# Kernel tuning notes

Hardware: AMD Instinct MI355X
Metric: run time of the kernel (lower is better)

## Reference

```python
import jax, jax.numpy as jnp
import numpy as np

N, T, D, H = 4, 2048, 512, 8
HD = D // H  # head dim = split size


def setup_inputs() -> dict:
    key = jax.random.key(0)
    k1, k2, k3, k4 = jax.random.split(key, 4)
    scale = 1.0 / np.sqrt(D)
    return {
        "query": jax.random.normal(k1, (N, T, D), dtype=jnp.float32),
        "Wk": jax.random.normal(k2, (D, D), dtype=jnp.float32) * scale,
        "Wv": jax.random.normal(k3, (D, D), dtype=jnp.float32) * scale,
        "Wo": jax.random.normal(k4, (D, D), dtype=jnp.float32) * scale,
    }


def reference(query, Wk, Wv, Wo):
    # torch.nn.Linear(x) == x @ W.T (no bias)
    querys = query                              # [N, T, D]
    keys = query @ Wk.T + query                 # residual-added keys [N, T, D]
    values = query @ Wv.T                       # [N, T, D]

    # split along feature dim into H heads, stacked on a leading head axis
    def split_heads(x):
        # [N, T, D] -> [H, N, T, HD]
        return jnp.transpose(x.reshape(N, T, H, HD), (2, 0, 1, 3))

    q = split_heads(querys)
    k = split_heads(keys)
    v = split_heads(values)

    scores = jnp.einsum("hnqd,hnkd->hnqk", q, k) / np.sqrt(HD).astype(np.float32)
    scores = jax.nn.softmax(scores, axis=3)      # [H, N, Tq, Tk]
    out = jnp.einsum("hnqk,hnkd->hnqd", scores, v)

    # concat heads back along feature dim: [H, N, T, HD] -> [N, T, D]
    out = jnp.transpose(out, (1, 2, 0, 3)).reshape(N, T, D)
    out = out @ Wo.T
    return out
```

## Files before the change

### kernel.cpp

```cpp
#include <hip/hip_runtime.h>
#include <cstdint>
#include <cstddef>

#define NB 4
#define TS 2048
#define DM 512
#define HN 8
#define HD 64

typedef __attribute__((ext_vector_type(8))) short bf16x8;
typedef __attribute__((ext_vector_type(16))) float f32x16;
typedef __attribute__((ext_vector_type(4))) float f32x4;
typedef __attribute__((ext_vector_type(4))) short short4v;
typedef __attribute__((ext_vector_type(4))) unsigned u32x4;

static __device__ __forceinline__ short f2bf(float f) {
  unsigned u = __float_as_uint(f);
  unsigned r = (u + 0x7fffu + ((u >> 16) & 1u)) >> 16;
  return (short)r;
}

static __device__ __forceinline__ float bf2f(short s) {
  return __uint_as_float(((unsigned)(unsigned short)s) << 16);
}

static __device__ __forceinline__ unsigned cvtpk(float lo, float hi) {
  unsigned r;
  asm("v_cvt_pk_bf16_f32 %0, %1, %2" : "=v"(r) : "v"(lo), "v"(hi));
  return r;
}

static __device__ __forceinline__ void plane32swap(unsigned& x, unsigned& y) {
  asm volatile("v_permlane32_swap_b32 %0, %1" : "+v"(x), "+v"(y));
}

static __device__ __forceinline__ void gload16(const void* g, void* l) {
  __builtin_amdgcn_global_load_lds(
      (const __attribute__((address_space(1))) void*)g,
      (__attribute__((address_space(3))) void*)l, 16, 0, 0);
}

#define WAIT_VM(N) asm volatile("s_waitcnt vmcnt(" #N ")" ::: "memory")
#define BAR() __builtin_amdgcn_s_barrier()

#define MFMA16(a, b, c) __builtin_amdgcn_mfma_f32_16x16x32_bf16((a), (b), (c), 0, 0, 0)
#define MFMA32(a, b, c) __builtin_amdgcn_mfma_f32_32x32x16_bf16((a), (b), (c), 0, 0, 0)

__global__ __launch_bounds__(256) void cast_all(const float* __restrict__ Q,
                                                const float* __restrict__ Wk,
                                                const float* __restrict__ Wv,
                                                const float* __restrict__ Wo,
                                                short* __restrict__ Qb,
                                                short* __restrict__ Wb) {
  int i = blockIdx.x * 256 + threadIdx.x;
  const int Q4 = (NB * TS * DM) / 4;
  const float* src;
  short* dst;
  int off;
  int which = -1;
  if (i < Q4) {
    src = Q; dst = Qb; off = i;
  } else {
    int j = i - Q4;
    which = j >> 16;
    off = j & 65535;
    src = which == 0 ? Wk : (which == 1 ? Wv : Wo);
    dst = Wb + ((size_t)which << 18);
  }
  float4 v = reinterpret_cast<const float4*>(src)[off];
  if (which == 0) {
    int e0 = off * 4;
    int row = e0 >> 9;
    int col0 = e0 & 511;
    if (row >= col0 && row < col0 + 4) {
      int c = row - col0;
      if (c == 0) v.x += 1.0f;
      else if (c == 1) v.y += 1.0f;
      else if (c == 2) v.z += 1.0f;
      else v.w += 1.0f;
    }
  }
  short4v o;
  o.x = f2bf(v.x);
  o.y = f2bf(v.y);
  o.z = f2bf(v.z);
  o.w = f2bf(v.w);
  reinterpret_cast<short4v*>(dst)[off] = o;
}

__global__ __launch_bounds__(256) void gemm_kv(const short* __restrict__ Qb,
                                               const short* __restrict__ Wkb,
                                               const short* __restrict__ Wvb,
                                               short* __restrict__ KP,
                                               short* __restrict__ VP) {
  __shared__ alignas(16) short lA[2][128 * 32];
  __shared__ alignas(16) short lK[2][64 * 32];
  __shared__ alignas(16) short lV[2][64 * 32];
  const int row0 = blockIdx.x * 128;
  const int col0d = blockIdx.y * 64;
  const int tid = threadIdx.x;
  const int lane = tid & 63;
  const int wave = tid >> 6;
  const int wr = wave >> 1, wc = wave & 1;
  const int fr = lane & 15, fk = (lane >> 4) * 8;
  const int g = lane >> 4;

  f32x4 kacc[2][4], vacc[4][2];
  const f32x4 z4 = {0.f, 0.f, 0.f, 0.f};
#pragma unroll
  for (int m = 0; m < 4; ++m)
#pragma unroll
    for (int nn = 0; nn < 2; ++nn) {
      kacc[nn][m] = z4;
      vacc[m][nn] = z4;
    }

  const int sr = tid >> 2;
  const int sc8 = (tid & 3) * 8;

#define GSTAGE(buf, kt)                                                 \
  do {                                                                  \
    gload16(&Qb[(size_t)(row0 + sr) * DM + (kt) + sc8],                 \
            (char*)&lA[(buf)][0] + (size_t)tid * 16);                   \
    gload16(&Qb[(size_t)(row0 + 64 + sr) * DM + (kt) + sc8],            \
            (char*)&lA[(buf)][0] + 4096 + (size_t)tid * 16);            \
    gload16(&Wkb[(size_t)(col0d + sr) * DM + (kt) + sc8],               \
            (char*)&lK[(buf)][0] + (size_t)tid * 16);                   \
    gload16(&Wvb[(size_t)(col0d + sr) * DM + (kt) + sc8],               \
            (char*)&lV[(buf)][0] + (size_t)tid * 16);                   \
  } while (0)

  GSTAGE(0, 0);
  __syncthreads();
  int cur = 0;
  for (int kt = 0; kt < 16; ++kt) {
    if (kt < 15) GSTAGE(cur ^ 1, (kt + 1) * 32);
    bf16x8 af[4], wk[2], wv[2];
#pragma unroll
    for (int m = 0; m < 4; ++m)
      af[m] = *reinterpret_cast<const bf16x8*>(&lA[cur][(wr * 64 + m * 16 + fr) * 32 + fk]);
#pragma unroll
    for (int nn = 0; nn < 2; ++nn) {
      wk[nn] = *reinterpret_cast<const bf16x8*>(&lK[cur][(wc * 32 + nn * 16 + fr) * 32 + fk]);
      wv[nn] = *reinterpret_cast<const bf16x8*>(&lV[cur][(wc * 32 + nn * 16 + fr) * 32 + fk]);
    }
    __builtin_amdgcn_s_setprio(1);
#pragma unroll
    for (int m = 0; m < 4; ++m)
#pragma unroll
      for (int nn = 0; nn < 2; ++nn) {
        kacc[nn][m] = MFMA16(wk[nn], af[m], kacc[nn][m]);
        vacc[m][nn] = MFMA16(af[m], wv[nn], vacc[m][nn]);
      }
    __builtin_amdgcn_s_setprio(0);
    __syncthreads();
    cur ^= 1;
  }
#undef GSTAGE

#pragma unroll
  for (int nn = 0; nn < 2; ++nn) {
#pragma unroll
    for (int m = 0; m < 4; ++m) {
      int d = col0d + wc * 32 + nn * 16 + g * 4;
      int kseq = row0 + wr * 64 + m * 16 + fr;
      int h = d >> 6, dd = d & 63;
      int n = kseq >> 11, kk = kseq & (TS - 1);
      int t = kk >> 6, H = (kk >> 5) & 1;
      int ks = (dd >> 4) & 3, hfd = (dd >> 3) & 1, jb = dd & 7;
      int slot = (kk & 31) + 32 * hfd;
      short4v pk;
#pragma unroll
      for (int i = 0; i < 4; ++i) pk[i] = f2bf(kacc[nn][m][i]);
      size_t addr = ((((size_t)(n * HN + h) * 32 + t) * 8 + H * 4 + ks) * 64 + slot) * 8 + jb;
      *reinterpret_cast<short4v*>(&KP[addr]) = pk;
    }
  }
#pragma unroll
  for (int m = 0; m < 4; ++m) {
#pragma unroll
    for (int nn = 0; nn < 2; ++nn) {
      int kseq = row0 + wr * 64 + m * 16 + g * 4;
      int d = col0d + wc * 32 + nn * 16 + fr;
      int h = d >> 6, dd = d & 63;
      int n = kseq >> 11, kk = kseq & (TS - 1);
      int t = kk >> 6, hfk = (kk >> 3) & 1, jb = kk & 7;
      int ksV = (kk >> 4) & 3, D = (dd >> 5) & 1;
      int slot = (dd & 31) + 32 * hfk;
      short4v pv;
#pragma unroll
      for (int i = 0; i < 4; ++i) pv[i] = f2bf(vacc[m][nn][i]);
      size_t addr = ((((size_t)(n * HN + h) * 32 + t) * 8 + D * 4 + ksV) * 64 + slot) * 8 + jb;
      *reinterpret_cast<short4v*>(&VP[addr]) = pv;
    }
  }
}

__global__ __launch_bounds__(256) void gemm_o(const short* __restrict__ A,
                                              const short* __restrict__ W,
                                              float* __restrict__ out0) {
  __shared__ alignas(16) short lA[2][128 * 32];
  __shared__ alignas(16) short lB[2][64 * 32];
  const int row0 = blockIdx.x * 128;
  const int col0 = blockIdx.y * 64;
  const int tid = threadIdx.x;
  const int lane = tid & 63;
  const int wave = tid >> 6;
  const int wr = wave >> 1, wc = wave & 1;
  const int fr = lane & 15, fk = (lane >> 4) * 8;

  f32x4 acc[4][2];
  const f32x4 z4 = {0.f, 0.f, 0.f, 0.f};
#pragma unroll
  for (int m = 0; m < 4; ++m)
#pragma unroll
    for (int nn = 0; nn < 2; ++nn) acc[m][nn] = z4;

  const int sr = tid >> 2;
  const int sc8 = (tid & 3) * 8;

#define GSTAGE(buf, kt)                                                \
  do {                                                                 \
    gload16(&A[(size_t)(row0 + sr) * DM + (kt) + sc8],                 \
            (char*)&lA[(buf)][0] + (size_t)tid * 16);                  \
    gload16(&A[(size_t)(row0 + 64 + sr) * DM + (kt) + sc8],            \
            (char*)&lA[(buf)][0] + 4096 + (size_t)tid * 16);           \
    gload16(&W[(size_t)(col0 + sr) * DM + (kt) + sc8],                 \
            (char*)&lB[(buf)][0] + (size_t)tid * 16);                  \
  } while (0)

  GSTAGE(0, 0);
  __syncthreads();
  int cur = 0;
  for (int kt = 0; kt < 16; ++kt) {
    if (kt < 15) GSTAGE(cur ^ 1, (kt + 1) * 32);
    bf16x8 af[4], bfr[2];
#pragma unroll
    for (int m = 0; m < 4; ++m)
      af[m] = *reinterpret_cast<const bf16x8*>(&lA[cur][(wr * 64 + m * 16 + fr) * 32 + fk]);
#pragma unroll
    for (int nn = 0; nn < 2; ++nn)
      bfr[nn] = *reinterpret_cast<const bf16x8*>(&lB[cur][(wc * 32 + nn * 16 + fr) * 32 + fk]);
    __builtin_amdgcn_s_setprio(1);
#pragma unroll
    for (int m = 0; m < 4; ++m)
#pragma unroll
      for (int nn = 0; nn < 2; ++nn) acc[m][nn] = MFMA16(af[m], bfr[nn], acc[m][nn]);
    __builtin_amdgcn_s_setprio(0);
    __syncthreads();
    cur ^= 1;
  }
#undef GSTAGE

#pragma unroll
  for (int m = 0; m < 4; ++m)
#pragma unroll
    for (int nn = 0; nn < 2; ++nn)
#pragma unroll
      for (int i = 0; i < 4; ++i) {
        int gr = row0 + wr * 64 + m * 16 + (lane >> 4) * 4 + i;
        int gc = col0 + wc * 32 + nn * 16 + fr;
        out0[(size_t)gr * DM + gc] = acc[m][nn][i];
      }
}

__global__ __launch_bounds__(512, 4) void attn(const short* __restrict__ Qb,
                                               const short* __restrict__ KP,
                                               const short* __restrict__ VP,
                                               short* __restrict__ Ob) {
  __shared__ alignas(16) short kv[2][2][2][64 * 64];
  const int bid = blockIdx.x;
  const int blk = (bid & 7) * 64 + (bid >> 3);
  const int qt = blk & 15;
  const int nh = blk >> 4;
  const int h = nh & (HN - 1);
  const int n = nh >> 3;
  const int wv = threadIdx.x >> 6, lane = threadIdx.x & 63;
  const int grp = wv >> 2, qs = wv & 3;
  const int l31 = lane & 31, hf = lane >> 5;
  const int q0 = qt * 128 + qs * 32;
  const float SC2 = 0.18033688011f;

  bf16x8 qf[4];
  const short* qrow = Qb + (size_t)(n * TS + q0 + l31) * DM + h * HD;
#pragma unroll
  for (int ks = 0; ks < 4; ++ks) {
    bf16x8 t = *reinterpret_cast<const bf16x8*>(qrow + ks * 16 + hf * 8);
#pragma unroll
    for (int j = 0; j < 8; ++j) t[j] = f2bf(bf2f(t[j]) * SC2);
    qf[ks] = t;
  }

  bf16x8 ones;
#pragma unroll
  for (int i = 0; i < 8; ++i) ones[i] = (short)0x3F80;

  f32x16 o0, o1, osum;
#pragma unroll
  for (int r = 0; r < 16; ++r) {
    o0[r] = 0.f;
    o1[r] = 0.f;
    osum[r] = 0.f;
  }

  const int tbase = grp * 16;
  const size_t nhbase = (size_t)nh * 32 * 4096;

#define STAGE(buf, t)                                                           \
  do {                                                                          \
    const short* kS = KP + nhbase + (size_t)(t) * 4096 + qs * 1024 + lane * 8;  \
    const short* vS = VP + nhbase + (size_t)(t) * 4096 + qs * 1024 + lane * 8;  \
    char* kb_ = (char*)&kv[grp][(buf)][0][0] + qs * 2048;                       \
    char* vb_ = (char*)&kv[grp][(buf)][1][0] + qs * 2048;                       \
    gload16(kS, kb_);                                                           \
    gload16(kS + 512, kb_ + 1024);                                              \
    gload16(vS, vb_);                                                           \
    gload16(vS + 512, vb_ + 1024);                                              \
  } while (0)

  STAGE(0, tbase);

  const int lb = lane * 16;
  int cur = 0;
  for (int j = 0; j < 16; ++j) {
    if (j < 15) {
      STAGE(cur ^ 1, tbase + j + 1);
      WAIT_VM(4);
    } else {
      WAIT_VM(0);
    }
    BAR();

    const char* Kl = (const char*)&kv[grp][cur][0][0];
    const char* Vl = (const char*)&kv[grp][cur][1][0];

    f32x16 s0, s1;
#pragma unroll
    for (int r = 0; r < 16; ++r) {
      s0[r] = 0.f;
      s1[r] = 0.f;
    }
    __builtin_amdgcn_s_setprio(1);
#pragma unroll
    for (int ks = 0; ks < 4; ++ks) {
      bf16x8 ka0 = *reinterpret_cast<const bf16x8*>(Kl + ks * 1024 + lb);
      bf16x8 ka1 = *reinterpret_cast<const bf16x8*>(Kl + (4 + ks) * 1024 + lb);
      s0 = MFMA32(ka0, qf[ks], s0);
      s1 = MFMA32(ka1, qf[ks], s1);
    }
    __builtin_amdgcn_s_setprio(0);

#pragma unroll
    for (int r = 0; r < 16; ++r) {
      s0[r] = __builtin_amdgcn_exp2f(s0[r]);
      s1[r] = __builtin_amdgcn_exp2f(s1[r]);
    }

    unsigned w0[4][2], w1[4][2];
#pragma unroll
    for (int c = 0; c < 4; ++c) {
      w0[c][0] = cvtpk(s0[4 * c], s0[4 * c + 1]);
      w0[c][1] = cvtpk(s0[4 * c + 2], s0[4 * c + 3]);
      w1[c][0] = cvtpk(s1[4 * c], s1[4 * c + 1]);
      w1[c][1] = cvtpk(s1[4 * c + 2], s1[4 * c + 3]);
    }

    __builtin_amdgcn_s_setprio(1);
#pragma unroll
    for (int ks = 0; ks < 4; ++ks) {
      const int ce = (ks & 1) * 2, co = ce + 1;
      unsigned xa = (ks < 2) ? w0[ce][0] : w1[ce][0];
      unsigned xb = (ks < 2) ? w0[ce][1] : w1[ce][1];
      unsigned ya = (ks < 2) ? w0[co][0] : w1[co][0];
      unsigned yb = (ks < 2) ? w0[co][1] : w1[co][1];
      plane32swap(xa, ya);
      plane32swap(xb, yb);
      u32x4 pw;
      pw.x = xa;
      pw.y = xb;
      pw.z = ya;
      pw.w = yb;
      bf16x8 pa = *reinterpret_cast<bf16x8*>(&pw);

      bf16x8 v0 = *reinterpret_cast<const bf16x8*>(Vl + ks * 1024 + lb);
      bf16x8 v1 = *reinterpret_cast<const bf16x8*>(Vl + (4 + ks) * 1024 + lb);
      o0 = MFMA32(pa, v0, o0);
      o1 = MFMA32(pa, v1, o1);
      osum = MFMA32(pa, ones, osum);
    }
    __builtin_amdgcn_s_setprio(0);

    BAR();
    cur ^= 1;
  }
#undef STAGE

  float* sp = (float*)&kv[0][0][0][0];
  const int sbase = (qs * 64 + lane) * 49;
  if (grp == 1) {
#pragma unroll
    for (int r = 0; r < 16; ++r) {
      sp[sbase + r] = o0[r];
      sp[sbase + 16 + r] = o1[r];
      sp[sbase + 32 + r] = osum[r];
    }
  }
  __syncthreads();
  if (grp == 0) {
#pragma unroll
    for (int r = 0; r < 16; ++r) {
      o0[r] += sp[sbase + r];
      o1[r] += sp[sbase + 16 + r];
      osum[r] += sp[sbase + 32 + r];
    }
#pragma unroll
    for (int r = 0; r < 16; ++r) {
      int q = q0 + (r & 3) + 8 * (r >> 2) + 4 * hf;
      float is = 1.0f / osum[r];
      size_t base = (size_t)(n * TS + q) * DM + h * HD;
      Ob[base + l31] = f2bf(o0[r] * is);
      Ob[base + 32 + l31] = f2bf(o1[r] * is);
    }
  }
}

extern "C" void kernel_launch(void* const* d_in, const int* in_sizes, int n_in,
                              void* d_out, int out_size, void* d_ws, size_t ws_size,
                              hipStream_t stream) {
  (void)in_sizes; (void)n_in; (void)out_size; (void)ws_size;
  const float* Q = (const float*)d_in[0];
  const float* Wk = (const float*)d_in[1];
  const float* Wv = (const float*)d_in[2];
  const float* Wo = (const float*)d_in[3];

  const size_t QE = (size_t)NB * TS * DM;
  const size_t WE = (size_t)DM * DM;
  short* ws = (short*)d_ws;
  short* Qb = ws;
  short* KP = Qb + QE;
  short* VP = KP + QE;
  short* Ao = VP + QE;
  short* Wkb = Ao + QE;
  short* Wvb = Wkb + WE;
  short* Wob = Wvb + WE;

  {
    int total4 = (int)((QE + 3 * WE) / 4);
    cast_all<<<total4 / 256, 256, 0, stream>>>(Q, Wk, Wv, Wo, Qb, Wkb);
  }
  {
    dim3 g(64, 8);
    gemm_kv<<<g, 256, 0, stream>>>(Qb, Wkb, Wvb, KP, VP);
  }
  attn<<<NB * HN * (TS / 128), 512, 0, stream>>>(Qb, KP, VP, Ao);
  {
    dim3 g(64, 8);
    gemm_o<<<g, 256, 0, stream>>>(Ao, Wob, (float*)d_out);
  }
}
```

Before: 79.71 us.

## Halve row tiles in projection GEMMs and attention; single-buffer attention K/V

The K/V projection and output GEMMs now use 64-row tiles instead of 128-row tiles, which doubles their grid size. The attention kernel drops from 512 to 256 threads per block and covers 64 query rows per block instead of 128. Its K/V staging goes from a double-buffered prefetch to a single buffer that is loaded after each compute step. The goal is more blocks and lower LDS use per block, for better CU occupancy and balance. The cost is that K/V load latency is no longer overlapped with compute, and K/V and weight tiles are re-read more often from global memory.

```diff
diff --git a/kernel.cpp b/kernel.cpp
--- a/kernel.cpp
+++ b/kernel.cpp
@@ -93,10 +93,10 @@
                                                const short* __restrict__ Wvb,
                                                short* __restrict__ KP,
                                                short* __restrict__ VP) {
-  __shared__ alignas(16) short lA[2][128 * 32];
+  __shared__ alignas(16) short lA[2][64 * 32];
   __shared__ alignas(16) short lK[2][64 * 32];
   __shared__ alignas(16) short lV[2][64 * 32];
-  const int row0 = blockIdx.x * 128;
+  const int row0 = blockIdx.x * 64;
   const int col0d = blockIdx.y * 64;
   const int tid = threadIdx.x;
   const int lane = tid & 63;
@@ -105,10 +105,10 @@
   const int fr = lane & 15, fk = (lane >> 4) * 8;
   const int g = lane >> 4;
 
-  f32x4 kacc[2][4], vacc[4][2];
+  f32x4 kacc[2][2], vacc[2][2];
   const f32x4 z4 = {0.f, 0.f, 0.f, 0.f};
 #pragma unroll
-  for (int m = 0; m < 4; ++m)
+  for (int m = 0; m < 2; ++m)
 #pragma unroll
     for (int nn = 0; nn < 2; ++nn) {
       kacc[nn][m] = z4;
@@ -122,8 +122,6 @@
   do {                                                                  \
     gload16(&Qb[(size_t)(row0 + sr) * DM + (kt) + sc8],                 \
             (char*)&lA[(buf)][0] + (size_t)tid * 16);                   \
-    gload16(&Qb[(size_t)(row0 + 64 + sr) * DM + (kt) + sc8],            \
-            (char*)&lA[(buf)][0] + 4096 + (size_t)tid * 16);            \
     gload16(&Wkb[(size_t)(col0d + sr) * DM + (kt) + sc8],               \
             (char*)&lK[(buf)][0] + (size_t)tid * 16);                   \
     gload16(&Wvb[(size_t)(col0d + sr) * DM + (kt) + sc8],               \
@@ -135,10 +133,10 @@
   int cur = 0;
   for (int kt = 0; kt < 16; ++kt) {
     if (kt < 15) GSTAGE(cur ^ 1, (kt + 1) * 32);
-    bf16x8 af[4], wk[2], wv[2];
-#pragma unroll
-    for (int m = 0; m < 4; ++m)
-      af[m] = *reinterpret_cast<const bf16x8*>(&lA[cur][(wr * 64 + m * 16 + fr) * 32 + fk]);
+    bf16x8 af[2], wk[2], wv[2];
+#pragma unroll
+    for (int m = 0; m < 2; ++m)
+      af[m] = *reinterpret_cast<const bf16x8*>(&lA[cur][(wr * 32 + m * 16 + fr) * 32 + fk]);
 #pragma unroll
     for (int nn = 0; nn < 2; ++nn) {
       wk[nn] = *reinterpret_cast<const bf16x8*>(&lK[cur][(wc * 32 + nn * 16 + fr) * 32 + fk]);
@@ -146,7 +144,7 @@
     }
     __builtin_amdgcn_s_setprio(1);
 #pragma unroll
-    for (int m = 0; m < 4; ++m)
+    for (int m = 0; m < 2; ++m)
 #pragma unroll
       for (int nn = 0; nn < 2; ++nn) {
         kacc[nn][m] = MFMA16(wk[nn], af[m], kacc[nn][m]);
@@ -161,9 +159,9 @@
 #pragma unroll
   for (int nn = 0; nn < 2; ++nn) {
 #pragma unroll
-    for (int m = 0; m < 4; ++m) {
+    for (int m = 0; m < 2; ++m) {
       int d = col0d + wc * 32 + nn * 16 + g * 4;
-      int kseq = row0 + wr * 64 + m * 16 + fr;
+      int kseq = row0 + wr * 32 + m * 16 + fr;
       int h = d >> 6, dd = d & 63;
       int n = kseq >> 11, kk = kseq & (TS - 1);
       int t = kk >> 6, H = (kk >> 5) & 1;
@@ -177,10 +175,10 @@
     }
   }
 #pragma unroll
-  for (int m = 0; m < 4; ++m) {
+  for (int m = 0; m < 2; ++m) {
 #pragma unroll
     for (int nn = 0; nn < 2; ++nn) {
-      int kseq = row0 + wr * 64 + m * 16 + g * 4;
+      int kseq = row0 + wr * 32 + m * 16 + g * 4;
       int d = col0d + wc * 32 + nn * 16 + fr;
       int h = d >> 6, dd = d & 63;
       int n = kseq >> 11, kk = kseq & (TS - 1);
@@ -199,9 +197,9 @@
 __global__ __launch_bounds__(256) void gemm_o(const short* __restrict__ A,
                                               const short* __restrict__ W,
                                               float* __restrict__ out0) {
-  __shared__ alignas(16) short lA[2][128 * 32];
+  __shared__ alignas(16) short lA[2][64 * 32];
   __shared__ alignas(16) short lB[2][64 * 32];
-  const int row0 = blockIdx.x * 128;
+  const int row0 = blockIdx.x * 64;
   const int col0 = blockIdx.y * 64;
   const int tid = threadIdx.x;
   const int lane = tid & 63;
@@ -209,10 +207,10 @@
   const int wr = wave >> 1, wc = wave & 1;
   const int fr = lane & 15, fk = (lane >> 4) * 8;
 
-  f32x4 acc[4][2];
+  f32x4 acc[2][2];
   const f32x4 z4 = {0.f, 0.f, 0.f, 0.f};
 #pragma unroll
-  for (int m = 0; m < 4; ++m)
+  for (int m = 0; m < 2; ++m)
 #pragma unroll
     for (int nn = 0; nn < 2; ++nn) acc[m][nn] = z4;
 
@@ -223,8 +221,6 @@
   do {                                                                 \
     gload16(&A[(size_t)(row0 + sr) * DM + (kt) + sc8],                 \
             (char*)&lA[(buf)][0] + (size_t)tid * 16);                  \
-    gload16(&A[(size_t)(row0 + 64 + sr) * DM + (kt) + sc8],            \
-            (char*)&lA[(buf)][0] + 4096 + (size_t)tid * 16);           \
     gload16(&W[(size_t)(col0 + sr) * DM + (kt) + sc8],                 \
             (char*)&lB[(buf)][0] + (size_t)tid * 16);                  \
   } while (0)
@@ -234,16 +230,16 @@
   int cur = 0;
   for (int kt = 0; kt < 16; ++kt) {
     if (kt < 15) GSTAGE(cur ^ 1, (kt + 1) * 32);
-    bf16x8 af[4], bfr[2];
-#pragma unroll
-    for (int m = 0; m < 4; ++m)
-      af[m] = *reinterpret_cast<const bf16x8*>(&lA[cur][(wr * 64 + m * 16 + fr) * 32 + fk]);
+    bf16x8 af[2], bfr[2];
+#pragma unroll
+    for (int m = 0; m < 2; ++m)
+      af[m] = *reinterpret_cast<const bf16x8*>(&lA[cur][(wr * 32 + m * 16 + fr) * 32 + fk]);
 #pragma unroll
     for (int nn = 0; nn < 2; ++nn)
       bfr[nn] = *reinterpret_cast<const bf16x8*>(&lB[cur][(wc * 32 + nn * 16 + fr) * 32 + fk]);
     __builtin_amdgcn_s_setprio(1);
 #pragma unroll
-    for (int m = 0; m < 4; ++m)
+    for (int m = 0; m < 2; ++m)
 #pragma unroll
       for (int nn = 0; nn < 2; ++nn) acc[m][nn] = MFMA16(af[m], bfr[nn], acc[m][nn]);
     __builtin_amdgcn_s_setprio(0);
@@ -253,32 +249,32 @@
 #undef GSTAGE
 
 #pragma unroll
-  for (int m = 0; m < 4; ++m)
+  for (int m = 0; m < 2; ++m)
 #pragma unroll
     for (int nn = 0; nn < 2; ++nn)
 #pragma unroll
       for (int i = 0; i < 4; ++i) {
-        int gr = row0 + wr * 64 + m * 16 + (lane >> 4) * 4 + i;
+        int gr = row0 + wr * 32 + m * 16 + (lane >> 4) * 4 + i;
         int gc = col0 + wc * 32 + nn * 16 + fr;
         out0[(size_t)gr * DM + gc] = acc[m][nn][i];
       }
 }
 
-__global__ __launch_bounds__(512, 4) void attn(const short* __restrict__ Qb,
+__global__ __launch_bounds__(256, 4) void attn(const short* __restrict__ Qb,
                                                const short* __restrict__ KP,
                                                const short* __restrict__ VP,
                                                short* __restrict__ Ob) {
-  __shared__ alignas(16) short kv[2][2][2][64 * 64];
+  __shared__ alignas(16) short kv[2][2][4096];
   const int bid = blockIdx.x;
-  const int blk = (bid & 7) * 64 + (bid >> 3);
-  const int qt = blk & 15;
-  const int nh = blk >> 4;
+  const int blk = (bid & 7) * 128 + (bid >> 3);
+  const int qt = blk & 31;
+  const int nh = blk >> 5;
   const int h = nh & (HN - 1);
   const int n = nh >> 3;
   const int wv = threadIdx.x >> 6, lane = threadIdx.x & 63;
-  const int grp = wv >> 2, qs = wv & 3;
+  const int grp = wv >> 1, qs = wv & 1;
   const int l31 = lane & 31, hf = lane >> 5;
-  const int q0 = qt * 128 + qs * 32;
+  const int q0 = qt * 64 + qs * 32;
   const float SC2 = 0.18033688011f;
 
   bf16x8 qf[4];
@@ -306,33 +302,31 @@
   const int tbase = grp * 16;
   const size_t nhbase = (size_t)nh * 32 * 4096;
 
-#define STAGE(buf, t)                                                           \
+#define STAGE(t)                                                                \
   do {                                                                          \
-    const short* kS = KP + nhbase + (size_t)(t) * 4096 + qs * 1024 + lane * 8;  \
-    const short* vS = VP + nhbase + (size_t)(t) * 4096 + qs * 1024 + lane * 8;  \
-    char* kb_ = (char*)&kv[grp][(buf)][0][0] + qs * 2048;                       \
-    char* vb_ = (char*)&kv[grp][(buf)][1][0] + qs * 2048;                       \
+    const short* kS = KP + nhbase + (size_t)(t) * 4096 + qs * 2048 + lane * 8;  \
+    const short* vS = VP + nhbase + (size_t)(t) * 4096 + qs * 2048 + lane * 8;  \
+    char* kb_ = (char*)&kv[grp][0][0] + qs * 4096;                              \
+    char* vb_ = (char*)&kv[grp][1][0] + qs * 4096;                              \
     gload16(kS, kb_);                                                           \
     gload16(kS + 512, kb_ + 1024);                                              \
+    gload16(kS + 1024, kb_ + 2048);                                             \
+    gload16(kS + 1536, kb_ + 3072);                                             \
     gload16(vS, vb_);                                                           \
     gload16(vS + 512, vb_ + 1024);                                              \
+    gload16(vS + 1024, vb_ + 2048);                                             \
+    gload16(vS + 1536, vb_ + 3072);                                             \
   } while (0)
 
-  STAGE(0, tbase);
+  STAGE(tbase);
 
   const int lb = lane * 16;
-  int cur = 0;
   for (int j = 0; j < 16; ++j) {
-    if (j < 15) {
-      STAGE(cur ^ 1, tbase + j + 1);
-      WAIT_VM(4);
-    } else {
-      WAIT_VM(0);
-    }
+    WAIT_VM(0);
     BAR();
 
-    const char* Kl = (const char*)&kv[grp][cur][0][0];
-    const char* Vl = (const char*)&kv[grp][cur][1][0];
+    const char* Kl = (const char*)&kv[grp][0][0];
+    const char* Vl = (const char*)&kv[grp][1][0];
 
     f32x16 s0, s1;
 #pragma unroll
@@ -391,11 +385,11 @@
     __builtin_amdgcn_s_setprio(0);
 
     BAR();
-    cur ^= 1;
+    if (j < 15) STAGE(tbase + j + 1);
   }
 #undef STAGE
 
-  float* sp = (float*)&kv[0][0][0][0];
+  float* sp = (float*)&kv[0][0][0];
   const int sbase = (qs * 64 + lane) * 49;
   if (grp == 1) {
 #pragma unroll
@@ -449,12 +443,12 @@
     cast_all<<<total4 / 256, 256, 0, stream>>>(Q, Wk, Wv, Wo, Qb, Wkb);
   }
   {
-    dim3 g(64, 8);
+    dim3 g(128, 8);
     gemm_kv<<<g, 256, 0, stream>>>(Qb, Wkb, Wvb, KP, VP);
   }
-  attn<<<NB * HN * (TS / 128), 512, 0, stream>>>(Qb, KP, VP, Ao);
+  attn<<<NB * HN * (TS / 64), 256, 0, stream>>>(Qb, KP, VP, Ao);
   {
-    dim3 g(64, 8);
+    dim3 g(128, 8);
     gemm_o<<<g, 256, 0, stream>>>(Ao, Wob, (float*)d_out);
   }
 }
```

Result: slower. 87.31 us (+9.5%).

## Software-pipeline attention loop: overlap QK of next tile with PV of previous

Applied to the files above, without the earlier changes.

Restructures the attention inner loop so that each iteration computes QK^T for tile j while doing the PV product for tile j-1 using probabilities packed in the previous iteration. K and V are now staged separately with staggered prefetch, K one tile ahead and V aligned to the PV step, and the LDS buffers are reindexed accordingly. The aim is to let the exp/pack work overlap with MFMA work and to shorten the dependency chain between QK, softmax and PV. This adds a prologue and epilogue, keeps more live registers (cw arrays and s0/s1 across iterations), and makes the vmcnt wait counts more delicate.

```diff
diff --git a/kernel.cpp b/kernel.cpp
--- a/kernel.cpp
+++ b/kernel.cpp
@@ -268,7 +268,7 @@
                                                const short* __restrict__ KP,
                                                const short* __restrict__ VP,
                                                short* __restrict__ Ob) {
-  __shared__ alignas(16) short kv[2][2][2][64 * 64];
+  __shared__ alignas(16) short kv[2][2][2][4096];
   const int bid = blockIdx.x;
   const int blk = (bid & 7) * 64 + (bid >> 3);
   const int qt = blk & 15;
@@ -295,105 +295,128 @@
 #pragma unroll
   for (int i = 0; i < 8; ++i) ones[i] = (short)0x3F80;
 
-  f32x16 o0, o1, osum;
+  f32x16 o0, o1, osum, s0, s1;
 #pragma unroll
   for (int r = 0; r < 16; ++r) {
     o0[r] = 0.f;
     o1[r] = 0.f;
     osum[r] = 0.f;
   }
+  unsigned cw0[4][2], cw1[4][2];
 
   const int tbase = grp * 16;
   const size_t nhbase = (size_t)nh * 32 * 4096;
-
-#define STAGE(buf, t)                                                           \
-  do {                                                                          \
-    const short* kS = KP + nhbase + (size_t)(t) * 4096 + qs * 1024 + lane * 8;  \
-    const short* vS = VP + nhbase + (size_t)(t) * 4096 + qs * 1024 + lane * 8;  \
-    char* kb_ = (char*)&kv[grp][(buf)][0][0] + qs * 2048;                       \
-    char* vb_ = (char*)&kv[grp][(buf)][1][0] + qs * 2048;                       \
-    gload16(kS, kb_);                                                           \
-    gload16(kS + 512, kb_ + 1024);                                              \
-    gload16(vS, vb_);                                                           \
-    gload16(vS + 512, vb_ + 1024);                                              \
-  } while (0)
-
-  STAGE(0, tbase);
-
   const int lb = lane * 16;
-  int cur = 0;
-  for (int j = 0; j < 16; ++j) {
-    if (j < 15) {
-      STAGE(cur ^ 1, tbase + j + 1);
-      WAIT_VM(4);
-    } else {
-      WAIT_VM(0);
-    }
+
+#define STAGE_K(buf, t)                                                          \
+  do {                                                                           \
+    const short* kS = KP + nhbase + (size_t)(t) * 4096 + qs * 1024 + lane * 8;   \
+    char* kb_ = (char*)&kv[grp][0][(buf)][0] + qs * 2048;                        \
+    gload16(kS, kb_);                                                            \
+    gload16(kS + 512, kb_ + 1024);                                               \
+  } while (0)
+
+#define STAGE_V(buf, t)                                                          \
+  do {                                                                           \
+    const short* vS = VP + nhbase + (size_t)(t) * 4096 + qs * 1024 + lane * 8;   \
+    char* vb_ = (char*)&kv[grp][1][(buf)][0] + qs * 2048;                        \
+    gload16(vS, vb_);                                                            \
+    gload16(vS + 512, vb_ + 1024);                                               \
+  } while (0)
+
+#define QK_BODY(par)                                                             \
+  do {                                                                           \
+    const char* Kl = (const char*)&kv[grp][0][(par)][0];                         \
+    _Pragma("unroll") for (int r = 0; r < 16; ++r) {                             \
+      s0[r] = 0.f;                                                               \
+      s1[r] = 0.f;                                                               \
+    }                                                                            \
+    __builtin_amdgcn_s_setprio(1);                                               \
+    _Pragma("unroll") for (int ks = 0; ks < 4; ++ks) {                           \
+      bf16x8 ka0 = *reinterpret_cast<const bf16x8*>(Kl + ks * 1024 + lb);        \
+      bf16x8 ka1 = *reinterpret_cast<const bf16x8*>(Kl + (4 + ks) * 1024 + lb);  \
+      s0 = MFMA32(ka0, qf[ks], s0);                                              \
+      s1 = MFMA32(ka1, qf[ks], s1);                                              \
+    }                                                                            \
+    __builtin_amdgcn_s_setprio(0);                                               \
+  } while (0)
+
+#define PV_BODY(par)                                                             \
+  do {                                                                           \
+    const char* Vl = (const char*)&kv[grp][1][(par)][0];                         \
+    __builtin_amdgcn_s_setprio(1);                                               \
+    _Pragma("unroll") for (int ks = 0; ks < 4; ++ks) {                           \
+      const int ce = (ks & 1) * 2, co = ce + 1;                                  \
+      unsigned xa = (ks < 2) ? cw0[ce][0] : cw1[ce][0];                          \
+      unsigned xb = (ks < 2) ? cw0[ce][1] : cw1[ce][1];                          \
+      unsigned ya = (ks < 2) ? cw0[co][0] : cw1[co][0];                          \
+      unsigned yb = (ks < 2) ? cw0[co][1] : cw1[co][1];                          \
+      plane32swap(xa, ya);                                                       \
+      plane32swap(xb, yb);                                                       \
+      u32x4 pw;                                                                  \
+      pw.x = xa;                                                                 \
+      pw.y = xb;                                                                 \
+      pw.z = ya;                                                                 \
+      pw.w = yb;                                                                 \
+      bf16x8 pa = *reinterpret_cast<bf16x8*>(&pw);                               \
+      bf16x8 v0 = *reinterpret_cast<const bf16x8*>(Vl + ks * 1024 + lb);         \
+      bf16x8 v1 = *reinterpret_cast<const bf16x8*>(Vl + (4 + ks) * 1024 + lb);   \
+      o0 = MFMA32(pa, v0, o0);                                                   \
+      o1 = MFMA32(pa, v1, o1);                                                   \
+      osum = MFMA32(pa, ones, osum);                                             \
+    }                                                                            \
+    __builtin_amdgcn_s_setprio(0);                                               \
+  } while (0)
+
+#define EXPPACK                                                                  \
+  do {                                                                           \
+    _Pragma("unroll") for (int r = 0; r < 16; ++r) {                             \
+      s0[r] = __builtin_amdgcn_exp2f(s0[r]);                                     \
+      s1[r] = __builtin_amdgcn_exp2f(s1[r]);                                     \
+    }                                                                            \
+    _Pragma("unroll") for (int c = 0; c < 4; ++c) {                              \
+      cw0[c][0] = cvtpk(s0[4 * c], s0[4 * c + 1]);                               \
+      cw0[c][1] = cvtpk(s0[4 * c + 2], s0[4 * c + 3]);                           \
+      cw1[c][0] = cvtpk(s1[4 * c], s1[4 * c + 1]);                               \
+      cw1[c][1] = cvtpk(s1[4 * c + 2], s1[4 * c + 3]);                           \
+    }                                                                            \
+  } while (0)
+
+  STAGE_K(0, tbase);
+  STAGE_K(1, tbase + 1);
+  STAGE_V(0, tbase);
+  WAIT_VM(4);
+  BAR();
+  QK_BODY(0);
+  EXPPACK;
+  BAR();
+  for (int j = 1; j < 15; ++j) {
+    STAGE_K((j + 1) & 1, tbase + j + 1);
+    STAGE_V(j & 1, tbase + j);
+    WAIT_VM(4);
     BAR();
-
-    const char* Kl = (const char*)&kv[grp][cur][0][0];
-    const char* Vl = (const char*)&kv[grp][cur][1][0];
-
-    f32x16 s0, s1;
-#pragma unroll
-    for (int r = 0; r < 16; ++r) {
-      s0[r] = 0.f;
-      s1[r] = 0.f;
-    }
-    __builtin_amdgcn_s_setprio(1);
-#pragma unroll
-    for (int ks = 0; ks < 4; ++ks) {
-      bf16x8 ka0 = *reinterpret_cast<const bf16x8*>(Kl + ks * 1024 + lb);
-      bf16x8 ka1 = *reinterpret_cast<const bf16x8*>(Kl + (4 + ks) * 1024 + lb);
-      s0 = MFMA32(ka0, qf[ks], s0);
-      s1 = MFMA32(ka1, qf[ks], s1);
-    }
-    __builtin_amdgcn_s_setprio(0);
-
-#pragma unroll
-    for (int r = 0; r < 16; ++r) {
-      s0[r] = __builtin_amdgcn_exp2f(s0[r]);
-      s1[r] = __builtin_amdgcn_exp2f(s1[r]);
-    }
-
-    unsigned w0[4][2], w1[4][2];
-#pragma unroll
-    for (int c = 0; c < 4; ++c) {
-      w0[c][0] = cvtpk(s0[4 * c], s0[4 * c + 1]);
-      w0[c][1] = cvtpk(s0[4 * c + 2], s0[4 * c + 3]);
-      w1[c][0] = cvtpk(s1[4 * c], s1[4 * c + 1]);
-      w1[c][1] = cvtpk(s1[4 * c + 2], s1[4 * c + 3]);
-    }
-
-    __builtin_amdgcn_s_setprio(1);
-#pragma unroll
-    for (int ks = 0; ks < 4; ++ks) {
-      const int ce = (ks & 1) * 2, co = ce + 1;
-      unsigned xa = (ks < 2) ? w0[ce][0] : w1[ce][0];
-      unsigned xb = (ks < 2) ? w0[ce][1] : w1[ce][1];
-      unsigned ya = (ks < 2) ? w0[co][0] : w1[co][0];
-      unsigned yb = (ks < 2) ? w0[co][1] : w1[co][1];
-      plane32swap(xa, ya);
-      plane32swap(xb, yb);
-      u32x4 pw;
-      pw.x = xa;
-      pw.y = xb;
-      pw.z = ya;
-      pw.w = yb;
-      bf16x8 pa = *reinterpret_cast<bf16x8*>(&pw);
-
-      bf16x8 v0 = *reinterpret_cast<const bf16x8*>(Vl + ks * 1024 + lb);
-      bf16x8 v1 = *reinterpret_cast<const bf16x8*>(Vl + (4 + ks) * 1024 + lb);
-      o0 = MFMA32(pa, v0, o0);
-      o1 = MFMA32(pa, v1, o1);
-      osum = MFMA32(pa, ones, osum);
-    }
-    __builtin_amdgcn_s_setprio(0);
-
+    QK_BODY(j & 1);
+    PV_BODY((j + 1) & 1);
+    EXPPACK;
     BAR();
-    cur ^= 1;
-  }
-#undef STAGE
+  }
+  STAGE_V(1, tbase + 15);
+  WAIT_VM(2);
+  BAR();
+  QK_BODY(1);
+  PV_BODY(0);
+  EXPPACK;
+  BAR();
+  WAIT_VM(0);
+  BAR();
+  PV_BODY(1);
+  BAR();
+
+#undef STAGE_K
+#undef STAGE_V
+#undef QK_BODY
+#undef PV_BODY
+#undef EXPPACK
 
   float* sp = (float*)&kv[0][0][0][0];
   const int sbase = (qs * 64 + lane) * 49;
```

After: 179.1 us. 2.25x slower.

## Load V fragments directly to registers and replace ones-MFMA rowsum with scalar sums

Applied to the files above, without the earlier changes.

Only K tiles are now staged through LDS. Each wave loads its V fragments straight from global memory into registers each iteration, which shrinks LDS use and removes the LDS reads for V. The softmax denominator was an extra MFMA against a vector of ones; it is now accumulated from the fp32 exp values in VALU adds, reduced across lanes with a shuffle, and broadcast per row with __shfl. In exchange, each V tile is fetched from global once per wave rather than once per workgroup, register pressure rises, and the row sums are taken before the bf16 rounding that the weights get.

```diff
diff --git a/kernel.cpp b/kernel.cpp
--- a/kernel.cpp
+++ b/kernel.cpp
@@ -268,7 +268,7 @@
                                                const short* __restrict__ KP,
                                                const short* __restrict__ VP,
                                                short* __restrict__ Ob) {
-  __shared__ alignas(16) short kv[2][2][2][64 * 64];
+  __shared__ alignas(16) short kv[2][2][4224];
   const int bid = blockIdx.x;
   const int blk = (bid & 7) * 64 + (bid >> 3);
   const int qt = blk & 15;
@@ -291,50 +291,45 @@
     qf[ks] = t;
   }
 
-  bf16x8 ones;
-#pragma unroll
-  for (int i = 0; i < 8; ++i) ones[i] = (short)0x3F80;
-
-  f32x16 o0, o1, osum;
+  f32x16 o0, o1, s0, s1;
 #pragma unroll
   for (int r = 0; r < 16; ++r) {
     o0[r] = 0.f;
     o1[r] = 0.f;
-    osum[r] = 0.f;
-  }
+  }
+  float rs[4] = {0.f, 0.f, 0.f, 0.f};
 
   const int tbase = grp * 16;
   const size_t nhbase = (size_t)nh * 32 * 4096;
-
-#define STAGE(buf, t)                                                           \
-  do {                                                                          \
-    const short* kS = KP + nhbase + (size_t)(t) * 4096 + qs * 1024 + lane * 8;  \
-    const short* vS = VP + nhbase + (size_t)(t) * 4096 + qs * 1024 + lane * 8;  \
-    char* kb_ = (char*)&kv[grp][(buf)][0][0] + qs * 2048;                       \
-    char* vb_ = (char*)&kv[grp][(buf)][1][0] + qs * 2048;                       \
-    gload16(kS, kb_);                                                           \
-    gload16(kS + 512, kb_ + 1024);                                              \
-    gload16(vS, vb_);                                                           \
-    gload16(vS + 512, vb_ + 1024);                                              \
+  const int lb = lane * 16;
+
+#define STAGE_K(buf, t)                                                          \
+  do {                                                                           \
+    const short* kS = KP + nhbase + (size_t)(t) * 4096 + qs * 1024 + lane * 8;   \
+    char* kb_ = (char*)&kv[grp][(buf)][0] + qs * 2048;                           \
+    gload16(kS, kb_);                                                            \
+    gload16(kS + 512, kb_ + 1024);                                               \
   } while (0)
 
-  STAGE(0, tbase);
-
-  const int lb = lane * 16;
+  STAGE_K(0, tbase);
+
   int cur = 0;
   for (int j = 0; j < 16; ++j) {
+    bf16x8 vf[8];
+    const short* vS = VP + nhbase + (size_t)(tbase + j) * 4096 + lane * 8;
+#pragma unroll
+    for (int b = 0; b < 8; ++b)
+      vf[b] = *reinterpret_cast<const bf16x8*>(vS + b * 512);
+
     if (j < 15) {
-      STAGE(cur ^ 1, tbase + j + 1);
-      WAIT_VM(4);
+      STAGE_K(cur ^ 1, tbase + j + 1);
+      WAIT_VM(10);
     } else {
-      WAIT_VM(0);
+      WAIT_VM(8);
     }
     BAR();
 
-    const char* Kl = (const char*)&kv[grp][cur][0][0];
-    const char* Vl = (const char*)&kv[grp][cur][1][0];
-
-    f32x16 s0, s1;
+    const char* Kl = (const char*)&kv[grp][cur][0];
 #pragma unroll
     for (int r = 0; r < 16; ++r) {
       s0[r] = 0.f;
@@ -355,7 +350,8 @@
       s0[r] = __builtin_amdgcn_exp2f(s0[r]);
       s1[r] = __builtin_amdgcn_exp2f(s1[r]);
     }
-
+#pragma unroll
+    for (int r = 0; r < 16; ++r) rs[r & 3] += s0[r] + s1[r];
     unsigned w0[4][2], w1[4][2];
 #pragma unroll
     for (int c = 0; c < 4; ++c) {
@@ -381,29 +377,28 @@
       pw.z = ya;
       pw.w = yb;
       bf16x8 pa = *reinterpret_cast<bf16x8*>(&pw);
-
-      bf16x8 v0 = *reinterpret_cast<const bf16x8*>(Vl + ks * 1024 + lb);
-      bf16x8 v1 = *reinterpret_cast<const bf16x8*>(Vl + (4 + ks) * 1024 + lb);
-      o0 = MFMA32(pa, v0, o0);
-      o1 = MFMA32(pa, v1, o1);
-      osum = MFMA32(pa, ones, osum);
+      o0 = MFMA32(pa, vf[ks], o0);
+      o1 = MFMA32(pa, vf[4 + ks], o1);
     }
     __builtin_amdgcn_s_setprio(0);
 
     BAR();
     cur ^= 1;
   }
-#undef STAGE
-
-  float* sp = (float*)&kv[0][0][0][0];
-  const int sbase = (qs * 64 + lane) * 49;
+#undef STAGE_K
+
+  float rst = (rs[0] + rs[1]) + (rs[2] + rs[3]);
+  rst += __shfl_xor(rst, 32);
+
+  float* sp = (float*)&kv[0][0][0];
+  const int sbase = (qs * 64 + lane) * 33;
   if (grp == 1) {
 #pragma unroll
     for (int r = 0; r < 16; ++r) {
       sp[sbase + r] = o0[r];
       sp[sbase + 16 + r] = o1[r];
-      sp[sbase + 32 + r] = osum[r];
-    }
+    }
+    sp[sbase + 32] = rst;
   }
   __syncthreads();
   if (grp == 0) {
@@ -411,12 +406,14 @@
     for (int r = 0; r < 16; ++r) {
       o0[r] += sp[sbase + r];
       o1[r] += sp[sbase + 16 + r];
-      osum[r] += sp[sbase + 32 + r];
-    }
+    }
+    rst += sp[sbase + 32];
+    float invv = 1.0f / rst;
 #pragma unroll
     for (int r = 0; r < 16; ++r) {
-      int q = q0 + (r & 3) + 8 * (r >> 2) + 4 * hf;
-      float is = 1.0f / osum[r];
+      int crow = (r & 3) + 8 * (r >> 2) + 4 * hf;
+      float is = __shfl(invv, crow);
+      int q = q0 + crow;
       size_t base = (size_t)(n * TS + q) * DM + h * HD;
       Ob[base + l31] = f2bf(o0[r] * is);
       Ob[base + 32 + l31] = f2bf(o1[r] * is);
```

New measurement: 84.81 us. 1.06x slower.
